# Kernel optimization log

Measured on AMD Instinct MI355X. Metric: run time of the kernel, lower is better.

Reference implementation:

```python
import jax, jax.numpy as jnp
import numpy as np

C_ATOM = 128
N_HEADS = 4
HEAD_DIM = C_ATOM // N_HEADS
B, L, A = 16, 2048, 4  # batch, residues, atoms per residue


def setup_inputs() -> dict:
    key = jax.random.key(0)
    ks = jax.random.split(key, 10)
    s = 1.0 / np.sqrt(C_ATOM)
    x = jax.random.normal(ks[0], (B, L, A, C_ATOM), dtype=jnp.float32)
    mask = jax.random.bernoulli(ks[1], 0.9, (B, L, A))
    def lin(kw, kb):
        W = jax.random.uniform(kw, (C_ATOM, C_ATOM), jnp.float32, -s, s)
        b = jax.random.uniform(kb, (C_ATOM,), jnp.float32, -s, s)
        return W, b
    Wq, bq = lin(ks[2], ks[3])
    Wk, bk = lin(ks[4], ks[5])
    Wv, bv = lin(ks[6], ks[7])
    Wo, bo = lin(ks[8], ks[9])
    return {"x": x, "mask": mask, "Wq": Wq, "bq": bq, "Wk": Wk, "bk": bk,
            "Wv": Wv, "bv": bv, "Wo": Wo, "bo": bo}


def reference(x, mask, Wq, bq, Wk, bk, Wv, bv, Wo, bo):
    B_, L_, A_, C = x.shape
    H, D = N_HEADS, HEAD_DIM
    scale = D ** -0.5

    def split_heads(t):  # (B,L,A,C) -> (B,L,H,A,D)
        return t.reshape(B_, L_, A_, H, D).transpose(0, 1, 3, 2, 4)

    q = split_heads(x @ Wq + bq)
    k = split_heads(x @ Wk + bk)
    v = split_heads(x @ Wv + bv)

    # per-residue 4x4 attention scores: (B,L,H,A,A)
    attn = jnp.einsum('blhad,blhed->blhae', q, k) * scale
    # mask keys: mask -> (B,L,1,1,A)
    attn = jnp.where(mask[:, :, None, None, :], attn, -jnp.inf)
    attn = jax.nn.softmax(attn, axis=-1)
    attn = jnp.where(jnp.isnan(attn), 0.0, attn)  # rows with all keys masked

    out = jnp.einsum('blhae,blhed->blhad', attn, v)
    out = out.transpose(0, 1, 3, 2, 4).reshape(B_, L_, A_, C)
    out = out @ Wo + bo
    # zero out residues with no valid atoms
    residue_mask = jnp.any(mask, axis=-1)[..., None, None]  # (B,L,1,1)
    out = out * residue_mask.astype(out.dtype)
    return out
```

## Files before the change

### kernel.cpp

```cpp
#include <hip/hip_runtime.h>
#include <hip/hip_bf16.h>

using f32x4  = __attribute__((ext_vector_type(4))) float;
using bf16x8 = __attribute__((ext_vector_type(8))) short;
typedef unsigned int u32;

__device__ __forceinline__ unsigned short f2bf(float f) {
  u32 u = __float_as_uint(f);
  u += 0x7FFFu + ((u >> 16) & 1u);
  return (unsigned short)(u >> 16);
}

__global__ __launch_bounds__(256) void cvt_weights(
    const float* __restrict__ Wq, const float* __restrict__ Wk,
    const float* __restrict__ Wv, const float* __restrict__ Wo,
    unsigned short* __restrict__ wsT)
{
  const int o = blockIdx.x * 256 + threadIdx.x;
  const int j   = o & 7;
  const int col = (o >> 3) & 127;
  const int blk = o >> 10;
  const int kk  = blk >> 2;
  const int gg  = blk & 3;
  const int src = (32 * kk + 8 * gg + j) * 128 + col;
  wsT[o]             = f2bf(Wq[src]);
  wsT[16384 + o]     = f2bf(Wk[src]);
  wsT[32768 + o]     = f2bf(Wv[src]);
  wsT[49152 + o]     = f2bf(Wo[src]);
}

__global__ __launch_bounds__(256) void laa_fused(
    const float* __restrict__ x, const void* __restrict__ maskp,
    const unsigned short* __restrict__ wsT,
    const float* __restrict__ bq, const float* __restrict__ bk,
    const float* __restrict__ bv, const float* __restrict__ bo,
    float* __restrict__ out, int n_tiles)
{
  constexpr int C = 128;
  __shared__ __align__(128) unsigned short Qlds[16 * 128];
  __shared__ __align__(128) unsigned short Klds[16 * 128];
  __shared__ __align__(128) unsigned short VTlds[128 * 24];
  __shared__ __align__(128) unsigned short Olds[2][16 * 128];

  const int tid  = threadIdx.x;
  const int wave = tid >> 6;
  const int lane = tid & 63;
  const int c0   = lane & 15;
  const int g    = lane >> 4;

  const u32* mw = (const u32*)maskp;
  u32 det = 0;
  #pragma unroll
  for (int i = 0; i < 64; ++i) det |= mw[i];
  const bool mask_is_byte = (det & 0xFFFFFF00u) != 0u;
  const unsigned char* mb = (const unsigned char*)maskp;
  const int mshift = mask_is_byte ? 0 : 2;

  bf16x8 wqf[2][4], wkf[2][4], wvf[2][4], wof[2][4];
  float bq2[2], bk2[2], bv2[2], bo2[2];
  #pragma unroll
  for (int t = 0; t < 2; ++t) {
    const int col = 16 * (2 * wave + t) + c0;
    bq2[t] = bq[col]; bk2[t] = bk[col]; bv2[t] = bv[col]; bo2[t] = bo[col];
    #pragma unroll
    for (int kk = 0; kk < 4; ++kk) {
      const int off = (kk * 4 + g) * 1024 + col * 8;
      wqf[t][kk] = *(const bf16x8*)(wsT + off);
      wkf[t][kk] = *(const bf16x8*)(wsT + 16384 + off);
      wvf[t][kk] = *(const bf16x8*)(wsT + 32768 + off);
      wof[t][kk] = *(const bf16x8*)(wsT + 49152 + off);
    }
  }

  const float scale = 0.17677669529663687f;
  const int hch = 32 * wave;
  int par = 0;

  for (int tile = blockIdx.x; tile < n_tiles; tile += gridDim.x) {
    const int rowbase = tile * 16;
    const float* xt = x + (size_t)rowbase * C;

    bf16x8 af[4];
    #pragma unroll
    for (int kk = 0; kk < 4; ++kk) {
      const float4* p = reinterpret_cast<const float4*>(xt + c0 * C + 32 * kk + 8 * g);
      float4 u0 = p[0], u1 = p[1];
      bf16x8 a;
      a[0]=(short)f2bf(u0.x); a[1]=(short)f2bf(u0.y); a[2]=(short)f2bf(u0.z); a[3]=(short)f2bf(u0.w);
      a[4]=(short)f2bf(u1.x); a[5]=(short)f2bf(u1.y); a[6]=(short)f2bf(u1.z); a[7]=(short)f2bf(u1.w);
      af[kk] = a;
    }

    float kvf[4];
    #pragma unroll
    for (int i = 0; i < 4; ++i) {
      const int idx = rowbase + 4 * g + i;
      kvf[i] = (mb[(size_t)idx << mshift] != 0) ? 1.0f : 0.0f;
    }

    f32x4 qa[2], ka[2], va[2];
    #pragma unroll
    for (int t = 0; t < 2; ++t) {
      qa[t] = f32x4{bq2[t], bq2[t], bq2[t], bq2[t]};
      ka[t] = f32x4{bk2[t], bk2[t], bk2[t], bk2[t]};
      va[t] = f32x4{bv2[t], bv2[t], bv2[t], bv2[t]};
    }
    #pragma unroll
    for (int kk = 0; kk < 4; ++kk) {
      #pragma unroll
      for (int t = 0; t < 2; ++t) {
        qa[t] = __builtin_amdgcn_mfma_f32_16x16x32_bf16(af[kk], wqf[t][kk], qa[t], 0, 0, 0);
        ka[t] = __builtin_amdgcn_mfma_f32_16x16x32_bf16(af[kk], wkf[t][kk], ka[t], 0, 0, 0);
        va[t] = __builtin_amdgcn_mfma_f32_16x16x32_bf16(af[kk], wvf[t][kk], va[t], 0, 0, 0);
      }
    }

    #pragma unroll
    for (int t = 0; t < 2; ++t) {
      const int ch = 16 * (2 * wave + t) + c0;
      #pragma unroll
      for (int i = 0; i < 4; ++i) {
        const int row = 4 * g + i;
        const int off = (row * 256 + ch * 2) ^ ((row & 7) << 4);
        *(unsigned short*)((char*)Qlds + off) = f2bf(qa[t][i] * scale);
        *(unsigned short*)((char*)Klds + off) = f2bf(ka[t][i]);
        VTlds[ch * 24 + row] = f2bf(va[t][i]);
      }
    }

    bf16x8 kfrag, qfrag;
    {
      const int row = c0;
      const int chb = hch + 8 * g;
      const int off = (row * 256 + chb * 2) ^ ((row & 7) << 4);
      kfrag = *(const bf16x8*)((const char*)Klds + off);
      qfrag = *(const bf16x8*)((const char*)Qlds + off);
    }
    f32x4 stv = f32x4{0.f, 0.f, 0.f, 0.f};
    stv = __builtin_amdgcn_mfma_f32_16x16x32_bf16(kfrag, qfrag, stv, 0, 0, 0);

    float mx = -1e30f;
    #pragma unroll
    for (int i = 0; i < 4; ++i) if (kvf[i] > 0.f) mx = fmaxf(mx, stv[i]);
    float p[4]; float den = 0.f;
    #pragma unroll
    for (int i = 0; i < 4; ++i) {
      p[i] = (kvf[i] > 0.f && mx > -1e29f) ? __expf(stv[i] - mx) : 0.f;
      den += p[i];
    }
    const float inv = den > 0.f ? 1.0f / den : 0.f;
    const bool diag = ((c0 >> 2) == g);
    u32 p01 = 0u, p23 = 0u;
    if (diag) {
      p01 = (u32)f2bf(p[0] * inv) | ((u32)f2bf(p[1] * inv) << 16);
      p23 = (u32)f2bf(p[2] * inv) | ((u32)f2bf(p[3] * inv) << 16);
    }

    const int srcA = ((2 * g) * 16 + c0) * 4;
    const int srcB = ((2 * g + 1) * 16 + c0) * 4;
    u32 w0 = (u32)__builtin_amdgcn_ds_bpermute(srcA, (int)p01);
    u32 w1 = (u32)__builtin_amdgcn_ds_bpermute(srcA, (int)p23);
    u32 w2 = (u32)__builtin_amdgcn_ds_bpermute(srcB, (int)p01);
    u32 w3 = (u32)__builtin_amdgcn_ds_bpermute(srcB, (int)p23);
    if (g >= 2) { w0 = 0u; w1 = 0u; w2 = 0u; w3 = 0u; }
    bf16x8 pfrag;
    pfrag[0] = (short)(w0 & 0xFFFFu); pfrag[1] = (short)(w0 >> 16);
    pfrag[2] = (short)(w1 & 0xFFFFu); pfrag[3] = (short)(w1 >> 16);
    pfrag[4] = (short)(w2 & 0xFFFFu); pfrag[5] = (short)(w2 >> 16);
    pfrag[6] = (short)(w3 & 0xFFFFu); pfrag[7] = (short)(w3 >> 16);

    f32x4 oa[2];
    oa[0] = f32x4{0.f,0.f,0.f,0.f}; oa[1] = f32x4{0.f,0.f,0.f,0.f};
    #pragma unroll
    for (int nt2 = 0; nt2 < 2; ++nt2) {
      bf16x8 vfrag;
      if (g < 2) {
        const int ch = hch + 16 * nt2 + c0;
        vfrag = *(const bf16x8*)(&VTlds[ch * 24 + 8 * g]);
      } else {
        vfrag[0]=0; vfrag[1]=0; vfrag[2]=0; vfrag[3]=0;
        vfrag[4]=0; vfrag[5]=0; vfrag[6]=0; vfrag[7]=0;
      }
      oa[nt2] = __builtin_amdgcn_mfma_f32_16x16x32_bf16(pfrag, vfrag, oa[nt2], 0, 0, 0);
    }

    unsigned short* Ob = &Olds[par][0];
    #pragma unroll
    for (int nt2 = 0; nt2 < 2; ++nt2) {
      const int ch = hch + 16 * nt2 + c0;
      #pragma unroll
      for (int i = 0; i < 4; ++i) {
        const int row = 4 * g + i;
        const int off = (row * 256 + ch * 2) ^ ((row & 7) << 4);
        *(unsigned short*)((char*)Ob + off) = f2bf(oa[nt2][i]);
      }
    }
    __syncthreads();

    bf16x8 of[4];
    #pragma unroll
    for (int kk = 0; kk < 4; ++kk) {
      const int row = c0;
      const int chb = 32 * kk + 8 * g;
      const int off = (row * 256 + chb * 2) ^ ((row & 7) << 4);
      of[kk] = *(const bf16x8*)((const char*)Ob + off);
    }
    f32x4 fa[2];
    #pragma unroll
    for (int t = 0; t < 2; ++t) fa[t] = f32x4{bo2[t], bo2[t], bo2[t], bo2[t]};
    #pragma unroll
    for (int kk = 0; kk < 4; ++kk) {
      #pragma unroll
      for (int t = 0; t < 2; ++t)
        fa[t] = __builtin_amdgcn_mfma_f32_16x16x32_bf16(of[kk], wof[t][kk], fa[t], 0, 0, 0);
    }

    const float rv = (kvf[0] + kvf[1] + kvf[2] + kvf[3]) > 0.f ? 1.0f : 0.f;
    #pragma unroll
    for (int t = 0; t < 2; ++t) {
      const int ch = 16 * (2 * wave + t) + c0;
      #pragma unroll
      for (int i = 0; i < 4; ++i) {
        const int row = rowbase + 4 * g + i;
        out[(size_t)row * C + ch] = fa[t][i] * rv;
      }
    }
    par ^= 1;
  }
}

extern "C" void kernel_launch(void* const* d_in, const int* in_sizes, int n_in,
                              void* d_out, int out_size, void* d_ws, size_t ws_size,
                              hipStream_t stream) {
  (void)n_in; (void)ws_size; (void)out_size;
  const float* x  = (const float*)d_in[0];
  const void* mask = d_in[1];
  const float* Wq = (const float*)d_in[2];
  const float* bq = (const float*)d_in[3];
  const float* Wk = (const float*)d_in[4];
  const float* bk = (const float*)d_in[5];
  const float* Wv = (const float*)d_in[6];
  const float* bv = (const float*)d_in[7];
  const float* Wo = (const float*)d_in[8];
  const float* bo = (const float*)d_in[9];
  float* out = (float*)d_out;
  unsigned short* wsT = (unsigned short*)d_ws;

  hipLaunchKernelGGL(cvt_weights, dim3(64), dim3(256), 0, stream, Wq, Wk, Wv, Wo, wsT);

  const int rows = in_sizes[0] / 128;
  const int n_tiles = rows / 16;
  int grid = n_tiles < 2048 ? n_tiles : 2048;
  hipLaunchKernelGGL(laa_fused, dim3(grid), dim3(256), 0, stream,
                     x, mask, wsT, bq, bk, bv, bo, out, n_tiles);
}
```

Before: 175.3 us.

## Assign one 16-row tile per wave and drop block-level synchronization

Work is split so each wave owns a whole 16-row tile and loops over the four heads, instead of four waves cooperating on one tile with a __syncthreads. Weights are no longer held in registers for the whole kernel; each head's Q/K/V weight fragments and the output-projection weights are reloaded from global/L2 per tile. This removes the block barrier and the heavy register footprint, which should raise occupancy. The cost is repeated weight loads on every tile and a serialized per-head loop inside each wave.

```diff
diff --git a/kernel.cpp b/kernel.cpp
--- a/kernel.cpp
+++ b/kernel.cpp
@@ -4,17 +4,18 @@
 using f32x4  = __attribute__((ext_vector_type(4))) float;
 using bf16x8 = __attribute__((ext_vector_type(8))) short;
 typedef unsigned int u32;
-
-__device__ __forceinline__ unsigned short f2bf(float f) {
+typedef unsigned short u16;
+
+__device__ __forceinline__ u16 f2bf(float f) {
   u32 u = __float_as_uint(f);
   u += 0x7FFFu + ((u >> 16) & 1u);
-  return (unsigned short)(u >> 16);
+  return (u16)(u >> 16);
 }
 
 __global__ __launch_bounds__(256) void cvt_weights(
     const float* __restrict__ Wq, const float* __restrict__ Wk,
     const float* __restrict__ Wv, const float* __restrict__ Wo,
-    unsigned short* __restrict__ wsT)
+    u16* __restrict__ wsT)
 {
   const int o = blockIdx.x * 256 + threadIdx.x;
   const int j   = o & 7;
@@ -23,24 +24,23 @@
   const int kk  = blk >> 2;
   const int gg  = blk & 3;
   const int src = (32 * kk + 8 * gg + j) * 128 + col;
-  wsT[o]             = f2bf(Wq[src]);
-  wsT[16384 + o]     = f2bf(Wk[src]);
-  wsT[32768 + o]     = f2bf(Wv[src]);
-  wsT[49152 + o]     = f2bf(Wo[src]);
-}
-
-__global__ __launch_bounds__(256) void laa_fused(
+  wsT[o]         = f2bf(Wq[src]);
+  wsT[16384 + o] = f2bf(Wk[src]);
+  wsT[32768 + o] = f2bf(Wv[src]);
+  wsT[49152 + o] = f2bf(Wo[src]);
+}
+
+__global__ __launch_bounds__(256) void laa_wave(
     const float* __restrict__ x, const void* __restrict__ maskp,
-    const unsigned short* __restrict__ wsT,
+    const u16* __restrict__ wsT,
     const float* __restrict__ bq, const float* __restrict__ bk,
     const float* __restrict__ bv, const float* __restrict__ bo,
     float* __restrict__ out, int n_tiles)
 {
-  constexpr int C = 128;
-  __shared__ __align__(128) unsigned short Qlds[16 * 128];
-  __shared__ __align__(128) unsigned short Klds[16 * 128];
-  __shared__ __align__(128) unsigned short VTlds[128 * 24];
-  __shared__ __align__(128) unsigned short Olds[2][16 * 128];
+  __shared__ __align__(16) u16 QhL[4][16 * 40];
+  __shared__ __align__(16) u16 KhL[4][16 * 40];
+  __shared__ __align__(16) u16 VTL[4][32 * 24];
+  __shared__ __align__(16) u16 OTL[4][16 * 128];
 
   const int tid  = threadIdx.x;
   const int wave = tid >> 6;
@@ -48,42 +48,26 @@
   const int c0   = lane & 15;
   const int g    = lane >> 4;
 
-  const u32* mw = (const u32*)maskp;
-  u32 det = 0;
-  #pragma unroll
-  for (int i = 0; i < 64; ++i) det |= mw[i];
-  const bool mask_is_byte = (det & 0xFFFFFF00u) != 0u;
+  u16* Qw = &QhL[wave][0];
+  u16* Kw = &KhL[wave][0];
+  u16* Vw = &VTL[wave][0];
+  u16* Ow = &OTL[wave][0];
+
+  const u32 mv0 = ((const u32*)maskp)[lane];
+  const bool mask_is_byte = __any((mv0 & 0xFFFFFF00u) != 0u);
   const unsigned char* mb = (const unsigned char*)maskp;
   const int mshift = mask_is_byte ? 0 : 2;
 
-  bf16x8 wqf[2][4], wkf[2][4], wvf[2][4], wof[2][4];
-  float bq2[2], bk2[2], bv2[2], bo2[2];
-  #pragma unroll
-  for (int t = 0; t < 2; ++t) {
-    const int col = 16 * (2 * wave + t) + c0;
-    bq2[t] = bq[col]; bk2[t] = bk[col]; bv2[t] = bv[col]; bo2[t] = bo[col];
-    #pragma unroll
-    for (int kk = 0; kk < 4; ++kk) {
-      const int off = (kk * 4 + g) * 1024 + col * 8;
-      wqf[t][kk] = *(const bf16x8*)(wsT + off);
-      wkf[t][kk] = *(const bf16x8*)(wsT + 16384 + off);
-      wvf[t][kk] = *(const bf16x8*)(wsT + 32768 + off);
-      wof[t][kk] = *(const bf16x8*)(wsT + 49152 + off);
-    }
-  }
-
   const float scale = 0.17677669529663687f;
-  const int hch = 32 * wave;
-  int par = 0;
-
-  for (int tile = blockIdx.x; tile < n_tiles; tile += gridDim.x) {
+
+  for (int tile = blockIdx.x * 4 + wave; tile < n_tiles; tile += (int)gridDim.x * 4) {
     const int rowbase = tile * 16;
-    const float* xt = x + (size_t)rowbase * C;
+    const float* xt = x + (size_t)rowbase * 128;
 
     bf16x8 af[4];
     #pragma unroll
     for (int kk = 0; kk < 4; ++kk) {
-      const float4* p = reinterpret_cast<const float4*>(xt + c0 * C + 32 * kk + 8 * g);
+      const float4* p = reinterpret_cast<const float4*>(xt + c0 * 128 + 32 * kk + 8 * g);
       float4 u0 = p[0], u1 = p[1];
       bf16x8 a;
       a[0]=(short)f2bf(u0.x); a[1]=(short)f2bf(u0.y); a[2]=(short)f2bf(u0.z); a[3]=(short)f2bf(u0.w);
@@ -98,134 +82,161 @@
       kvf[i] = (mb[(size_t)idx << mshift] != 0) ? 1.0f : 0.0f;
     }
 
-    f32x4 qa[2], ka[2], va[2];
-    #pragma unroll
-    for (int t = 0; t < 2; ++t) {
-      qa[t] = f32x4{bq2[t], bq2[t], bq2[t], bq2[t]};
-      ka[t] = f32x4{bk2[t], bk2[t], bk2[t], bk2[t]};
-      va[t] = f32x4{bv2[t], bv2[t], bv2[t], bv2[t]};
-    }
-    #pragma unroll
-    for (int kk = 0; kk < 4; ++kk) {
+    #pragma unroll 1
+    for (int h = 0; h < 4; ++h) {
+      const int cb = 32 * h;
+
+      f32x4 qa[2], ka[2], va[2];
+      {
+        bf16x8 w[2][4];
+        #pragma unroll
+        for (int t = 0; t < 2; ++t) {
+          const int col = cb + 16 * t + c0;
+          const float b = bq[col];
+          qa[t] = f32x4{b, b, b, b};
+          #pragma unroll
+          for (int kk = 0; kk < 4; ++kk)
+            w[t][kk] = *(const bf16x8*)(wsT + (kk * 4 + g) * 1024 + col * 8);
+        }
+        #pragma unroll
+        for (int kk = 0; kk < 4; ++kk)
+          #pragma unroll
+          for (int t = 0; t < 2; ++t)
+            qa[t] = __builtin_amdgcn_mfma_f32_16x16x32_bf16(af[kk], w[t][kk], qa[t], 0, 0, 0);
+      }
+      __builtin_amdgcn_sched_barrier(0);
+      {
+        bf16x8 w[2][4];
+        #pragma unroll
+        for (int t = 0; t < 2; ++t) {
+          const int col = cb + 16 * t + c0;
+          const float b = bk[col];
+          ka[t] = f32x4{b, b, b, b};
+          #pragma unroll
+          for (int kk = 0; kk < 4; ++kk)
+            w[t][kk] = *(const bf16x8*)(wsT + 16384 + (kk * 4 + g) * 1024 + col * 8);
+        }
+        #pragma unroll
+        for (int kk = 0; kk < 4; ++kk)
+          #pragma unroll
+          for (int t = 0; t < 2; ++t)
+            ka[t] = __builtin_amdgcn_mfma_f32_16x16x32_bf16(af[kk], w[t][kk], ka[t], 0, 0, 0);
+      }
+      __builtin_amdgcn_sched_barrier(0);
+      {
+        bf16x8 w[2][4];
+        #pragma unroll
+        for (int t = 0; t < 2; ++t) {
+          const int col = cb + 16 * t + c0;
+          const float b = bv[col];
+          va[t] = f32x4{b, b, b, b};
+          #pragma unroll
+          for (int kk = 0; kk < 4; ++kk)
+            w[t][kk] = *(const bf16x8*)(wsT + 32768 + (kk * 4 + g) * 1024 + col * 8);
+        }
+        #pragma unroll
+        for (int kk = 0; kk < 4; ++kk)
+          #pragma unroll
+          for (int t = 0; t < 2; ++t)
+            va[t] = __builtin_amdgcn_mfma_f32_16x16x32_bf16(af[kk], w[t][kk], va[t], 0, 0, 0);
+      }
+      __builtin_amdgcn_sched_barrier(0);
+
       #pragma unroll
       for (int t = 0; t < 2; ++t) {
-        qa[t] = __builtin_amdgcn_mfma_f32_16x16x32_bf16(af[kk], wqf[t][kk], qa[t], 0, 0, 0);
-        ka[t] = __builtin_amdgcn_mfma_f32_16x16x32_bf16(af[kk], wkf[t][kk], ka[t], 0, 0, 0);
-        va[t] = __builtin_amdgcn_mfma_f32_16x16x32_bf16(af[kk], wvf[t][kk], va[t], 0, 0, 0);
-      }
-    }
-
-    #pragma unroll
-    for (int t = 0; t < 2; ++t) {
-      const int ch = 16 * (2 * wave + t) + c0;
+        const int lch = 16 * t + c0;
+        #pragma unroll
+        for (int i = 0; i < 4; ++i) {
+          const int row = 4 * g + i;
+          Qw[row * 40 + lch] = f2bf(qa[t][i] * scale);
+          Kw[row * 40 + lch] = f2bf(ka[t][i]);
+          Vw[lch * 24 + row] = f2bf(va[t][i]);
+        }
+      }
+
+      bf16x8 kfrag = *(const bf16x8*)(Kw + c0 * 40 + 8 * g);
+      bf16x8 qfrag = *(const bf16x8*)(Qw + c0 * 40 + 8 * g);
+      f32x4 stv = f32x4{0.f, 0.f, 0.f, 0.f};
+      stv = __builtin_amdgcn_mfma_f32_16x16x32_bf16(kfrag, qfrag, stv, 0, 0, 0);
+
+      float mx = -1e30f;
+      #pragma unroll
+      for (int i = 0; i < 4; ++i) if (kvf[i] > 0.f) mx = fmaxf(mx, stv[i]);
+      float p[4]; float den = 0.f;
       #pragma unroll
       for (int i = 0; i < 4; ++i) {
-        const int row = 4 * g + i;
-        const int off = (row * 256 + ch * 2) ^ ((row & 7) << 4);
-        *(unsigned short*)((char*)Qlds + off) = f2bf(qa[t][i] * scale);
-        *(unsigned short*)((char*)Klds + off) = f2bf(ka[t][i]);
-        VTlds[ch * 24 + row] = f2bf(va[t][i]);
-      }
-    }
-
-    bf16x8 kfrag, qfrag;
-    {
-      const int row = c0;
-      const int chb = hch + 8 * g;
-      const int off = (row * 256 + chb * 2) ^ ((row & 7) << 4);
-      kfrag = *(const bf16x8*)((const char*)Klds + off);
-      qfrag = *(const bf16x8*)((const char*)Qlds + off);
-    }
-    f32x4 stv = f32x4{0.f, 0.f, 0.f, 0.f};
-    stv = __builtin_amdgcn_mfma_f32_16x16x32_bf16(kfrag, qfrag, stv, 0, 0, 0);
-
-    float mx = -1e30f;
-    #pragma unroll
-    for (int i = 0; i < 4; ++i) if (kvf[i] > 0.f) mx = fmaxf(mx, stv[i]);
-    float p[4]; float den = 0.f;
-    #pragma unroll
-    for (int i = 0; i < 4; ++i) {
-      p[i] = (kvf[i] > 0.f && mx > -1e29f) ? __expf(stv[i] - mx) : 0.f;
-      den += p[i];
-    }
-    const float inv = den > 0.f ? 1.0f / den : 0.f;
-    const bool diag = ((c0 >> 2) == g);
-    u32 p01 = 0u, p23 = 0u;
-    if (diag) {
-      p01 = (u32)f2bf(p[0] * inv) | ((u32)f2bf(p[1] * inv) << 16);
-      p23 = (u32)f2bf(p[2] * inv) | ((u32)f2bf(p[3] * inv) << 16);
-    }
-
-    const int srcA = ((2 * g) * 16 + c0) * 4;
-    const int srcB = ((2 * g + 1) * 16 + c0) * 4;
-    u32 w0 = (u32)__builtin_amdgcn_ds_bpermute(srcA, (int)p01);
-    u32 w1 = (u32)__builtin_amdgcn_ds_bpermute(srcA, (int)p23);
-    u32 w2 = (u32)__builtin_amdgcn_ds_bpermute(srcB, (int)p01);
-    u32 w3 = (u32)__builtin_amdgcn_ds_bpermute(srcB, (int)p23);
-    if (g >= 2) { w0 = 0u; w1 = 0u; w2 = 0u; w3 = 0u; }
-    bf16x8 pfrag;
-    pfrag[0] = (short)(w0 & 0xFFFFu); pfrag[1] = (short)(w0 >> 16);
-    pfrag[2] = (short)(w1 & 0xFFFFu); pfrag[3] = (short)(w1 >> 16);
-    pfrag[4] = (short)(w2 & 0xFFFFu); pfrag[5] = (short)(w2 >> 16);
-    pfrag[6] = (short)(w3 & 0xFFFFu); pfrag[7] = (short)(w3 >> 16);
-
-    f32x4 oa[2];
-    oa[0] = f32x4{0.f,0.f,0.f,0.f}; oa[1] = f32x4{0.f,0.f,0.f,0.f};
-    #pragma unroll
-    for (int nt2 = 0; nt2 < 2; ++nt2) {
-      bf16x8 vfrag;
-      if (g < 2) {
-        const int ch = hch + 16 * nt2 + c0;
-        vfrag = *(const bf16x8*)(&VTlds[ch * 24 + 8 * g]);
-      } else {
-        vfrag[0]=0; vfrag[1]=0; vfrag[2]=0; vfrag[3]=0;
-        vfrag[4]=0; vfrag[5]=0; vfrag[6]=0; vfrag[7]=0;
-      }
-      oa[nt2] = __builtin_amdgcn_mfma_f32_16x16x32_bf16(pfrag, vfrag, oa[nt2], 0, 0, 0);
-    }
-
-    unsigned short* Ob = &Olds[par][0];
-    #pragma unroll
-    for (int nt2 = 0; nt2 < 2; ++nt2) {
-      const int ch = hch + 16 * nt2 + c0;
-      #pragma unroll
-      for (int i = 0; i < 4; ++i) {
-        const int row = 4 * g + i;
-        const int off = (row * 256 + ch * 2) ^ ((row & 7) << 4);
-        *(unsigned short*)((char*)Ob + off) = f2bf(oa[nt2][i]);
-      }
-    }
-    __syncthreads();
+        p[i] = (kvf[i] > 0.f && mx > -1e29f) ? __expf(stv[i] - mx) : 0.f;
+        den += p[i];
+      }
+      const float inv = den > 0.f ? 1.0f / den : 0.f;
+      const bool diag = ((c0 >> 2) == g);
+      u32 p01 = 0u, p23 = 0u;
+      if (diag) {
+        p01 = (u32)f2bf(p[0] * inv) | ((u32)f2bf(p[1] * inv) << 16);
+        p23 = (u32)f2bf(p[2] * inv) | ((u32)f2bf(p[3] * inv) << 16);
+      }
+
+      const int srcA = ((2 * g) * 16 + c0) * 4;
+      const int srcB = ((2 * g + 1) * 16 + c0) * 4;
+      u32 w0 = (u32)__builtin_amdgcn_ds_bpermute(srcA, (int)p01);
+      u32 w1 = (u32)__builtin_amdgcn_ds_bpermute(srcA, (int)p23);
+      u32 w2 = (u32)__builtin_amdgcn_ds_bpermute(srcB, (int)p01);
+      u32 w3 = (u32)__builtin_amdgcn_ds_bpermute(srcB, (int)p23);
+      if (g >= 2) { w0 = 0u; w1 = 0u; w2 = 0u; w3 = 0u; }
+      bf16x8 pfrag;
+      pfrag[0] = (short)(w0 & 0xFFFFu); pfrag[1] = (short)(w0 >> 16);
+      pfrag[2] = (short)(w1 & 0xFFFFu); pfrag[3] = (short)(w1 >> 16);
+      pfrag[4] = (short)(w2 & 0xFFFFu); pfrag[5] = (short)(w2 >> 16);
+      pfrag[6] = (short)(w3 & 0xFFFFu); pfrag[7] = (short)(w3 >> 16);
+
+      #pragma unroll
+      for (int nt2 = 0; nt2 < 2; ++nt2) {
+        bf16x8 vfrag;
+        if (g < 2) {
+          vfrag = *(const bf16x8*)(Vw + (16 * nt2 + c0) * 24 + 8 * g);
+        } else {
+          vfrag[0]=0; vfrag[1]=0; vfrag[2]=0; vfrag[3]=0;
+          vfrag[4]=0; vfrag[5]=0; vfrag[6]=0; vfrag[7]=0;
+        }
+        f32x4 oa = f32x4{0.f, 0.f, 0.f, 0.f};
+        oa = __builtin_amdgcn_mfma_f32_16x16x32_bf16(pfrag, vfrag, oa, 0, 0, 0);
+        const int ch = cb + 16 * nt2 + c0;
+        #pragma unroll
+        for (int i = 0; i < 4; ++i) {
+          const int row = 4 * g + i;
+          const int off = (row * 256 + ch * 2) ^ ((row & 7) << 4);
+          *(u16*)((char*)Ow + off) = f2bf(oa[i]);
+        }
+      }
+      __builtin_amdgcn_sched_barrier(0);
+    }
 
     bf16x8 of[4];
     #pragma unroll
     for (int kk = 0; kk < 4; ++kk) {
-      const int row = c0;
-      const int chb = 32 * kk + 8 * g;
-      const int off = (row * 256 + chb * 2) ^ ((row & 7) << 4);
-      of[kk] = *(const bf16x8*)((const char*)Ob + off);
-    }
-    f32x4 fa[2];
-    #pragma unroll
-    for (int t = 0; t < 2; ++t) fa[t] = f32x4{bo2[t], bo2[t], bo2[t], bo2[t]};
-    #pragma unroll
-    for (int kk = 0; kk < 4; ++kk) {
-      #pragma unroll
-      for (int t = 0; t < 2; ++t)
-        fa[t] = __builtin_amdgcn_mfma_f32_16x16x32_bf16(of[kk], wof[t][kk], fa[t], 0, 0, 0);
-    }
-
+      const int off = (c0 * 256 + (32 * kk + 8 * g) * 2) ^ ((c0 & 7) << 4);
+      of[kk] = *(const bf16x8*)((const char*)Ow + off);
+    }
     const float rv = (kvf[0] + kvf[1] + kvf[2] + kvf[3]) > 0.f ? 1.0f : 0.f;
-    #pragma unroll
-    for (int t = 0; t < 2; ++t) {
-      const int ch = 16 * (2 * wave + t) + c0;
+
+    #pragma unroll 4
+    for (int colt = 0; colt < 8; ++colt) {
+      const int col = 16 * colt + c0;
+      const float b = bo[col];
+      bf16x8 w[4];
+      #pragma unroll
+      for (int kk = 0; kk < 4; ++kk)
+        w[kk] = *(const bf16x8*)(wsT + 49152 + (kk * 4 + g) * 1024 + col * 8);
+      f32x4 fa = f32x4{b, b, b, b};
+      #pragma unroll
+      for (int kk = 0; kk < 4; ++kk)
+        fa = __builtin_amdgcn_mfma_f32_16x16x32_bf16(of[kk], w[kk], fa, 0, 0, 0);
       #pragma unroll
       for (int i = 0; i < 4; ++i) {
         const int row = rowbase + 4 * g + i;
-        out[(size_t)row * C + ch] = fa[t][i] * rv;
-      }
-    }
-    par ^= 1;
+        out[(size_t)row * 128 + col] = fa[i] * rv;
+      }
+    }
   }
 }
 
@@ -244,13 +255,14 @@
   const float* Wo = (const float*)d_in[8];
   const float* bo = (const float*)d_in[9];
   float* out = (float*)d_out;
-  unsigned short* wsT = (unsigned short*)d_ws;
+  u16* wsT = (u16*)d_ws;
 
   hipLaunchKernelGGL(cvt_weights, dim3(64), dim3(256), 0, stream, Wq, Wk, Wv, Wo, wsT);
 
   const int rows = in_sizes[0] / 128;
   const int n_tiles = rows / 16;
-  int grid = n_tiles < 2048 ? n_tiles : 2048;
-  hipLaunchKernelGGL(laa_fused, dim3(grid), dim3(256), 0, stream,
+  const int wgs = (n_tiles + 3) / 4;
+  int grid = wgs < 2048 ? wgs : 2048;
+  hipLaunchKernelGGL(laa_wave, dim3(grid), dim3(256), 0, stream,
                      x, mask, wsT, bq, bk, bv, bo, out, n_tiles);
 }
```

New measurement: 164.3 us. -6.3%, faster.
